# Kernel optimization log

Measured on AMD Instinct MI355X. Metric: run time of the kernel, lower is better.

The kernel has to match this reference:

```python
import jax, jax.numpy as jnp
import numpy as np

EPS = 1e-6          # VN leaky-relu denominator eps (vn_layers.py)
NEG_SLOPE = 0.2     # VNLinearLeakyReLU default negative_slope
K = 3               # pointops.interpolation default k
DIST_EPS = 1e-8     # interpolation inverse-distance eps


def vn_linear_leakyrelu(x, w_feat, w_dir):
    # x: [B, Cin, 3, N]; w_*: [Cout, Cin]  (bias-free Linears over channel dim)
    p = jnp.einsum('oc,bcvn->bovn', w_feat, x)
    d = jnp.einsum('oc,bcvn->bovn', w_dir, x)
    dot = jnp.sum(p * d, axis=2, keepdims=True)          # [B,Cout,1,N]
    d2 = jnp.sum(d * d, axis=2, keepdims=True)
    mask = (dot >= 0).astype(x.dtype)
    proj = p - (dot / (d2 + EPS)) * d                    # reflect negative part onto plane perp to d
    return NEG_SLOPE * p + (1.0 - NEG_SLOPE) * (mask * p + (1.0 - mask) * proj)


def interpolation(p2, p1, feat, b, n2, n1):
    # p2: [b*n2,3] coarse coords, p1: [b*n1,3] fine coords, feat: [C,3,b*n2]
    # k-NN inverse-squared-distance interpolation, segment-local per cloud.
    C = feat.shape[0]
    p2b = p2.reshape(b, n2, 3)
    p1b = p1.reshape(b, n1, 3)
    featb = feat.reshape(C * 3, b, n2).transpose(1, 2, 0)  # [b, n2, C*3]

    def per_batch(q, s, f):
        d2 = jnp.sum((q[:, None, :] - s[None, :, :]) ** 2, axis=-1)  # [n1,n2]
        neg_d2, idx = jax.lax.top_k(-d2, K)                          # k smallest sq-dists
        w = 1.0 / (-neg_d2 + DIST_EPS)
        w = w / jnp.sum(w, axis=1, keepdims=True)                    # [n1,K]
        return jnp.einsum('nk,nkc->nc', w, f[idx])                   # [n1, C*3]

    out = jax.vmap(per_batch)(p1b, p2b, featb)                       # [b, n1, C*3]
    return out.reshape(b, n1, C, 3).transpose(2, 3, 0, 1).reshape(C, 3, b * n1)


def setup_inputs() -> dict:
    key = jax.random.key(0)
    ks = jax.random.split(key, 8)
    b, n1, n2 = 4, 16384, 4096
    in_planes, out_planes = 128, 64
    p1 = jax.random.uniform(ks[0], (b * n1, 3), dtype=jnp.float32)
    p2 = jax.random.uniform(ks[1], (b * n2, 3), dtype=jnp.float32)
    x1 = jax.random.normal(ks[2], (1, out_planes, 3, b * n1), dtype=jnp.float32)
    x2 = jax.random.normal(ks[3], (1, in_planes, 3, b * n2), dtype=jnp.float32)
    o1 = (jnp.arange(1, b + 1, dtype=jnp.int32)) * n1   # cumulative offsets
    o2 = (jnp.arange(1, b + 1, dtype=jnp.int32)) * n2
    s1 = 1.0 / np.sqrt(out_planes)
    s2 = 1.0 / np.sqrt(in_planes)
    w1_feat = jax.random.uniform(ks[4], (out_planes, out_planes), jnp.float32, -s1, s1)
    w1_dir = jax.random.uniform(ks[5], (out_planes, out_planes), jnp.float32, -s1, s1)
    w2_feat = jax.random.uniform(ks[6], (out_planes, in_planes), jnp.float32, -s2, s2)
    w2_dir = jax.random.uniform(ks[7], (out_planes, in_planes), jnp.float32, -s2, s2)
    return {"p1": p1, "x1": x1, "o1": o1, "p2": p2, "x2": x2, "o2": o2,
            "w1_feat": w1_feat, "w1_dir": w1_dir, "w2_feat": w2_feat, "w2_dir": w2_dir}


def reference(p1, x1, o1, p2, x2, o2, w1_feat, w1_dir, w2_feat, w2_dir):
    b = o1.shape[0]
    n1 = x1.shape[-1] // b
    n2 = x2.shape[-1] // b
    y1 = vn_linear_leakyrelu(x1, w1_feat, w1_dir)            # [1,Cout,3,N1]
    y2 = vn_linear_leakyrelu(x2, w2_feat, w2_dir)[0]         # squeeze(0) -> [Cout,3,N2]
    up = interpolation(p2, p1, y2, b, n2, n1)                # [Cout,3,N1]
    return y1 + up
```

## Files before the change

### kernel.cpp

```cpp
#include <hip/hip_runtime.h>

#define N1T 65536
#define N2T 16384
#define COUT 64
#define CH 192
#define GRD 8
#define HCELL 0.125f

typedef unsigned short bhalf;
typedef __attribute__((ext_vector_type(8))) short short8;
typedef __attribute__((ext_vector_type(4))) float f32x4;

__device__ __forceinline__ bhalf f2bf(float f) {
    unsigned u = __float_as_uint(f);
    return (bhalf)((u + 0x7FFFu + ((u >> 16) & 1u)) >> 16);
}
__device__ __forceinline__ float bf2f(bhalf h) {
    return __uint_as_float(((unsigned)h) << 16);
}

__global__ __launch_bounds__(256) void prep_kernel(
    const float* __restrict__ w1f, const float* __restrict__ w1d,
    const float* __restrict__ w2f, const float* __restrict__ w2d,
    bhalf* __restrict__ o1fh, bhalf* __restrict__ o1fl,
    bhalf* __restrict__ o1dh, bhalf* __restrict__ o1dl,
    bhalf* __restrict__ o2fh, bhalf* __restrict__ o2fl,
    bhalf* __restrict__ o2dh, bhalf* __restrict__ o2dl,
    int* __restrict__ zp) {
    if (blockIdx.x < 32) {
        const int i = blockIdx.x * 256 + threadIdx.x;
        if (i < 4096) {
            const float a = w1f[i]; const bhalf ah = f2bf(a);
            o1fh[i] = ah; o1fl[i] = f2bf(a - bf2f(ah));
            const float b = w1d[i]; const bhalf bh = f2bf(b);
            o1dh[i] = bh; o1dl[i] = f2bf(b - bf2f(bh));
        }
        const float a = w2f[i]; const bhalf ah = f2bf(a);
        o2fh[i] = ah; o2fl[i] = f2bf(a - bf2f(ah));
        const float b = w2d[i]; const bhalf bh = f2bf(b);
        o2dh[i] = bh; o2dl[i] = f2bf(b - bf2f(bh));
    } else {
        const int i = (blockIdx.x - 32) * 256 + threadIdx.x;
        if (i < 4096) zp[i] = 0;
    }
}

template<int CIN, int N, bool CM, int NT>
__global__ __launch_bounds__(512) void vn_mfma_kernel(
    const float* __restrict__ x,
    const bhalf* __restrict__ wfh, const bhalf* __restrict__ wfl,
    const bhalf* __restrict__ wdh, const bhalf* __restrict__ wdl,
    const int*   __restrict__ idxs,
    const float* __restrict__ wts,
    const float* __restrict__ y2t,
    float* __restrict__ out)
{
    constexpr int ROWS = CIN * 3;
    constexpr int LDSC = CIN * 3 + 8;
    constexpr int NB   = (NT > 1) ? 2 : 1;
    constexpr int NLD  = ROWS * 8 / 512;
    __shared__ __align__(16) bhalf xs_h[NB][32][LDSC];
    __shared__ __align__(16) bhalf xs_l[NB][32][LDSC];

    const int tid  = threadIdx.x;
    const int lane = tid & 63;
    const int wave = tid >> 6;
    const int r16  = lane & 15;
    const int hh   = lane >> 4;
    const int ot   = wave & 3;
    const int sW   = wave >> 2;
    const int pt   = sW * 16 + r16;
    const int tile0 = blockIdx.x * NT;

    int gk[NT][3]; float gw[NT][3];
    if constexpr (CM) {
#pragma unroll
        for (int t = 0; t < NT; ++t) {
            const int n = (tile0 + t) * 32 + pt;
#pragma unroll
            for (int r = 0; r < 3; ++r) {
                gk[t][r] = idxs[r * N1T + n];
                gw[t][r] = wts[r * N1T + n];
            }
        }
    }

    const int wofs = (ot * 16 + r16) * CIN + hh * 8;
    const bhalf* __restrict__ pfh = wfh + wofs;
    const bhalf* __restrict__ pfl = wfl + wofs;
    const bhalf* __restrict__ pdh = wdh + wofs;
    const bhalf* __restrict__ pdl = wdl + wofs;
    const int hs = ((hh ^ (r16 >> 2)) & 3) * 8;

    auto LOADT = [&](float4 (&st)[NLD], int t) {
#pragma unroll
        for (int r = 0; r < NLD; ++r) {
            const int i4 = r * 512 + tid;
            const int row = i4 >> 3, p4 = i4 & 7;
            st[r] = *(const float4*)&x[(size_t)row * N + (size_t)(tile0 + t) * 32 + p4 * 4];
        }
    };
    auto WRITET = [&](const float4 (&st)[NLD], int b) {
#pragma unroll
        for (int r = 0; r < NLD; ++r) {
            const int i4 = r * 512 + tid;
            const int row = i4 >> 3, p4 = i4 & 7;
            const int c = row / 3, vv = row - c * 3;
            const int colS = (vv * CIN + c) ^ ((p4 & 3) << 3);
            const float vals[4] = {st[r].x, st[r].y, st[r].z, st[r].w};
#pragma unroll
            for (int j = 0; j < 4; ++j) {
                const bhalf h = f2bf(vals[j]);
                xs_h[b][p4*4+j][colS] = h;
                xs_l[b][p4*4+j][colS] = f2bf(vals[j] - bf2f(h));
            }
        }
    };
    auto COMPUTET = [&](int t, int b, const int (&gkt)[3], const float (&gwt)[3]) {
        const f32x4 zero = {0.f, 0.f, 0.f, 0.f};
        f32x4 accP[3], accD[3];
#pragma unroll
        for (int v = 0; v < 3; ++v) { accP[v] = zero; accD[v] = zero; }
#pragma unroll
        for (int k = 0; k < CIN / 32; ++k) {
            const short8 afh = *(const short8*)(pfh + k * 32);
            const short8 afl = *(const short8*)(pfl + k * 32);
            const short8 adh = *(const short8*)(pdh + k * 32);
            const short8 adl = *(const short8*)(pdl + k * 32);
#pragma unroll
            for (int v = 0; v < 3; ++v) {
                const short8 bh = *(const short8*)&xs_h[b][pt][v * CIN + k * 32 + hs];
                const short8 bl = *(const short8*)&xs_l[b][pt][v * CIN + k * 32 + hs];
                accP[v] = __builtin_amdgcn_mfma_f32_16x16x32_bf16(afh, bh, accP[v], 0, 0, 0);
                accP[v] = __builtin_amdgcn_mfma_f32_16x16x32_bf16(afl, bh, accP[v], 0, 0, 0);
                accP[v] = __builtin_amdgcn_mfma_f32_16x16x32_bf16(afh, bl, accP[v], 0, 0, 0);
                accD[v] = __builtin_amdgcn_mfma_f32_16x16x32_bf16(adh, bh, accD[v], 0, 0, 0);
                accD[v] = __builtin_amdgcn_mfma_f32_16x16x32_bf16(adl, bh, accD[v], 0, 0, 0);
                accD[v] = __builtin_amdgcn_mfma_f32_16x16x32_bf16(adh, bl, accD[v], 0, 0, 0);
            }
        }
        float rr[12];
#pragma unroll
        for (int reg = 0; reg < 4; ++reg) {
            const float p0 = accP[0][reg], p1 = accP[1][reg], p2 = accP[2][reg];
            const float q0 = accD[0][reg], q1 = accD[1][reg], q2 = accD[2][reg];
            const float dot = p0*q0 + p1*q1 + p2*q2;
            const float dd  = q0*q0 + q1*q1 + q2*q2;
            const float coef = (dot < 0.f) ? (0.8f * dot / (dd + 1e-6f)) : 0.f;
            rr[reg*3+0] = p0 - coef * q0;
            rr[reg*3+1] = p1 - coef * q1;
            rr[reg*3+2] = p2 - coef * q2;
        }
        const int n = (tile0 + t) * 32 + pt;
        if constexpr (!CM) {
            float* op = out + (size_t)n * CH + ot * 48 + hh * 12;
            *(float4*)&op[0] = make_float4(rr[0], rr[1], rr[2],  rr[3]);
            *(float4*)&op[4] = make_float4(rr[4], rr[5], rr[6],  rr[7]);
            *(float4*)&op[8] = make_float4(rr[8], rr[9], rr[10], rr[11]);
        } else {
            const int chb = ot * 48 + hh * 12;
            const float* __restrict__ r0 = y2t + (size_t)gkt[0] * CH + chb;
            const float* __restrict__ r1 = y2t + (size_t)gkt[1] * CH + chb;
            const float* __restrict__ r2 = y2t + (size_t)gkt[2] * CH + chb;
            const float w0 = gwt[0], w1 = gwt[1], w2 = gwt[2];
            float4 a0[3], a1[3], a2[3];
#pragma unroll
            for (int q = 0; q < 3; ++q) {
                a0[q] = *(const float4*)&r0[q * 4];
                a1[q] = *(const float4*)&r1[q * 4];
                a2[q] = *(const float4*)&r2[q * 4];
            }
#pragma unroll
            for (int q = 0; q < 3; ++q) {
                const float u0 = w0*a0[q].x + w1*a1[q].x + w2*a2[q].x;
                const float u1 = w0*a0[q].y + w1*a1[q].y + w2*a2[q].y;
                const float u2 = w0*a0[q].z + w1*a1[q].z + w2*a2[q].z;
                const float u3 = w0*a0[q].w + w1*a1[q].w + w2*a2[q].w;
                out[(size_t)(chb + q*4 + 0) * N + n] = rr[q*4+0] + u0;
                out[(size_t)(chb + q*4 + 1) * N + n] = rr[q*4+1] + u1;
                out[(size_t)(chb + q*4 + 2) * N + n] = rr[q*4+2] + u2;
                out[(size_t)(chb + q*4 + 3) * N + n] = rr[q*4+3] + u3;
            }
        }
    };

    float4 stA[NLD], stB[NLD];
    LOADT(stA, 0);
    WRITET(stA, 0);
    if constexpr (NT == 2) {
        LOADT(stB, 1);
        __syncthreads();
        COMPUTET(0, 0, gk[0], gw[0]);
        WRITET(stB, 1);
        __syncthreads();
        COMPUTET(1, 1, gk[1], gw[1]);
    } else {
        __syncthreads();
        COMPUTET(0, 0, gk[0], gw[0]);
    }
}

#define KNN_INSERT(d2, j)                                        \
    {                                                            \
        const bool c0 = (d2) < b0;                               \
        const bool c1 = (d2) < b1;                               \
        const bool c2 = (d2) < b2v;                              \
        const float nb2 = c2 ? (c1 ? b1 : (d2)) : b2v;           \
        const int   ni2 = c2 ? (c1 ? i1 : (j))  : i2;            \
        const float nb1 = c1 ? (c0 ? b0 : (d2)) : b1;            \
        const int   ni1 = c1 ? (c0 ? i0 : (j))  : i1;            \
        b0 = c0 ? (d2) : b0;  i0 = c0 ? (j) : i0;                \
        b1 = nb1; i1 = ni1; b2v = nb2; i2 = ni2;                 \
    }

__device__ __forceinline__ int cell_of(float x, float y, float z) {
    int cx = (int)(x * (float)GRD); cx = cx < 0 ? 0 : (cx > GRD-1 ? GRD-1 : cx);
    int cy = (int)(y * (float)GRD); cy = cy < 0 ? 0 : (cy > GRD-1 ? GRD-1 : cy);
    int cz = (int)(z * (float)GRD); cz = cz < 0 ? 0 : (cz > GRD-1 ? GRD-1 : cz);
    return (cz << 6) | (cy << 3) | cx;
}

__global__ __launch_bounds__(256) void bin_count_kernel(
    const float* __restrict__ p2, int* __restrict__ counts) {
    const int i = blockIdx.x * 256 + threadIdx.x;
    const float x = p2[i*3+0], y = p2[i*3+1], z = p2[i*3+2];
    const int cell = ((i >> 12) << 9) | cell_of(x, y, z);
    atomicAdd(&counts[cell], 1);
}

__global__ __launch_bounds__(256) void scan_kernel(
    const int* __restrict__ counts, int* __restrict__ off) {
    __shared__ int buf[2][256];
    const int t = threadIdx.x;
    int v[8]; int s = 0;
#pragma unroll
    for (int j = 0; j < 8; ++j) { const int tmp = counts[t*8+j]; v[j] = s; s += tmp; }
    buf[0][t] = s; __syncthreads();
    int src = 0;
    for (int d = 1; d < 256; d <<= 1) {
        int val = buf[src][t];
        if (t >= d) val += buf[src][t - d];
        buf[src ^ 1][t] = val; src ^= 1; __syncthreads();
    }
    const int incl = buf[src][t];
    const int base = incl - s;
#pragma unroll
    for (int j = 0; j < 8; ++j) off[t*8+j] = base + v[j];
    if (t == 255) off[2048] = incl;
}

__global__ __launch_bounds__(256) void bin_scatter_kernel(
    const float* __restrict__ p2, const int* __restrict__ off,
    int* __restrict__ cnt2, float4* __restrict__ binned) {
    const int i = blockIdx.x * 256 + threadIdx.x;
    const float x = p2[i*3+0], y = p2[i*3+1], z = p2[i*3+2];
    const int cell = ((i >> 12) << 9) | cell_of(x, y, z);
    const int pos = off[cell] + atomicAdd(&cnt2[cell], 1);
    binned[pos] = make_float4(x, y, z, __int_as_float(i));
}

__global__ __launch_bounds__(512) void vn2_knn_kernel(
    const float* __restrict__ x2,
    const bhalf* __restrict__ wfh, const bhalf* __restrict__ wfl,
    const bhalf* __restrict__ wdh, const bhalf* __restrict__ wdl,
    float* __restrict__ y2t,
    const float* __restrict__ p1,
    const float4* __restrict__ binned,
    const int* __restrict__ off,
    int*   __restrict__ idx_out,
    float* __restrict__ w_out)
{
    constexpr int CIN = 128, N = N2T;
    constexpr int LDSC = CIN * 3 + 8;
    __shared__ __align__(16) bhalf xs_h[32][LDSC];
    __shared__ __align__(16) bhalf xs_l[32][LDSC];

    const int role = blockIdx.x & 1;
    const int ridx = blockIdx.x >> 1;
    const int tid  = threadIdx.x;

    if (role == 0) {
        const int lane = tid & 63;
        const int wave = tid >> 6;
        const int r16  = lane & 15;
        const int hh   = lane >> 4;
        const int ot   = wave & 3;
        const int sW   = wave >> 2;
        const int pt   = sW * 16 + r16;
        const int n0   = ridx * 32;

        const int wofs = (ot * 16 + r16) * CIN + hh * 8;
        const bhalf* __restrict__ pfh = wfh + wofs;
        const bhalf* __restrict__ pfl = wfl + wofs;
        const bhalf* __restrict__ pdh = wdh + wofs;
        const bhalf* __restrict__ pdl = wdl + wofs;
        const int hs = ((hh ^ (r16 >> 2)) & 3) * 8;

#pragma unroll
        for (int r = 0; r < 6; ++r) {
            const int i4 = r * 512 + tid;
            const int row = i4 >> 3, p4 = i4 & 7;
            const float4 v = *(const float4*)&x2[(size_t)row * N + n0 + p4 * 4];
            const int c = row / 3, vv = row - c * 3;
            const int colS = (vv * CIN + c) ^ ((p4 & 3) << 3);
            const float vals[4] = {v.x, v.y, v.z, v.w};
#pragma unroll
            for (int j = 0; j < 4; ++j) {
                const bhalf h = f2bf(vals[j]);
                xs_h[p4*4+j][colS] = h;
                xs_l[p4*4+j][colS] = f2bf(vals[j] - bf2f(h));
            }
        }
        __syncthreads();

        const f32x4 zero = {0.f, 0.f, 0.f, 0.f};
        f32x4 accP[3], accD[3];
#pragma unroll
        for (int v = 0; v < 3; ++v) { accP[v] = zero; accD[v] = zero; }
#pragma unroll
        for (int k = 0; k < CIN / 32; ++k) {
            const short8 afh = *(const short8*)(pfh + k * 32);
            const short8 afl = *(const short8*)(pfl + k * 32);
            const short8 adh = *(const short8*)(pdh + k * 32);
            const short8 adl = *(const short8*)(pdl + k * 32);
#pragma unroll
            for (int v = 0; v < 3; ++v) {
                const short8 bh = *(const short8*)&xs_h[pt][v * CIN + k * 32 + hs];
                const short8 bl = *(const short8*)&xs_l[pt][v * CIN + k * 32 + hs];
                accP[v] = __builtin_amdgcn_mfma_f32_16x16x32_bf16(afh, bh, accP[v], 0, 0, 0);
                accP[v] = __builtin_amdgcn_mfma_f32_16x16x32_bf16(afl, bh, accP[v], 0, 0, 0);
                accP[v] = __builtin_amdgcn_mfma_f32_16x16x32_bf16(afh, bl, accP[v], 0, 0, 0);
                accD[v] = __builtin_amdgcn_mfma_f32_16x16x32_bf16(adh, bh, accD[v], 0, 0, 0);
                accD[v] = __builtin_amdgcn_mfma_f32_16x16x32_bf16(adl, bh, accD[v], 0, 0, 0);
                accD[v] = __builtin_amdgcn_mfma_f32_16x16x32_bf16(adh, bl, accD[v], 0, 0, 0);
            }
        }

        float rr[12];
#pragma unroll
        for (int reg = 0; reg < 4; ++reg) {
            const float p0 = accP[0][reg], p1 = accP[1][reg], p2 = accP[2][reg];
            const float q0 = accD[0][reg], q1 = accD[1][reg], q2 = accD[2][reg];
            const float dot = p0*q0 + p1*q1 + p2*q2;
            const float dd  = q0*q0 + q1*q1 + q2*q2;
            const float coef = (dot < 0.f) ? (0.8f * dot / (dd + 1e-6f)) : 0.f;
            rr[reg*3+0] = p0 - coef * q0;
            rr[reg*3+1] = p1 - coef * q1;
            rr[reg*3+2] = p2 - coef * q2;
        }
        const int n = n0 + pt;
        float* op = y2t + (size_t)n * CH + ot * 48 + hh * 12;
        *(float4*)&op[0] = make_float4(rr[0], rr[1], rr[2],  rr[3]);
        *(float4*)&op[4] = make_float4(rr[4], rr[5], rr[6],  rr[7]);
        *(float4*)&op[8] = make_float4(rr[8], rr[9], rr[10], rr[11]);
    } else {
        const int fp  = ridx * 128 + (tid >> 2);
        const int sub = tid & 3;
        const int bi  = fp >> 14;
        const int cbase = bi << 9;

        const float qx = p1[fp*3+0], qy = p1[fp*3+1], qz = p1[fp*3+2];
        int cx = (int)(qx * (float)GRD); cx = cx < 0 ? 0 : (cx > 7 ? 7 : cx);
        int cy = (int)(qy * (float)GRD); cy = cy < 0 ? 0 : (cy > 7 ? 7 : cy);
        int cz = (int)(qz * (float)GRD); cz = cz < 0 ? 0 : (cz > 7 ? 7 : cz);

        const int x0 = cx > 0 ? cx - 1 : 0;
        const int x1 = cx < 7 ? cx + 1 : 7;

        float b0 = 1e30f, b1 = 1e30f, b2v = 1e30f;
        int   i0 = 0,     i1 = 0,     i2 = 0;

#pragma unroll
        for (int dz = -1; dz <= 1; ++dz) {
            const int nz = cz + dz;
            if ((unsigned)nz > 7u) continue;
#pragma unroll
            for (int dy = -1; dy <= 1; ++dy) {
                const int ny = cy + dy;
                if ((unsigned)ny > 7u) continue;
                const int cb = cbase + (nz << 6) + (ny << 3);
                const int s = off[cb + x0], e = off[cb + x1 + 1];
                for (int k = s + sub; k < e; k += 4) {
                    const float4 c4 = binned[k];
                    const float ddx = qx - c4.x, ddy = qy - c4.y, ddz = qz - c4.z;
                    const float d2 = fmaf(ddx, ddx, fmaf(ddy, ddy, ddz * ddz));
                    const int j = __float_as_int(c4.w);
                    KNN_INSERT(d2, j)
                }
            }
        }

#pragma unroll
        for (int m = 1; m <= 2; m <<= 1) {
            const float c0v = __shfl_xor(b0, m, 4);
            const float c1v = __shfl_xor(b1, m, 4);
            const float c2v = __shfl_xor(b2v, m, 4);
            const int   j0v = __shfl_xor(i0, m, 4);
            const int   j1v = __shfl_xor(i1, m, 4);
            const int   j2v = __shfl_xor(i2, m, 4);
            KNN_INSERT(c0v, j0v)
            KNN_INSERT(c1v, j1v)
            KNN_INSERT(c2v, j2v)
        }

        float dw = 1e30f;
        if (cx >= 2) dw = fminf(dw, qx - (float)(cx - 1) * HCELL);
        if (cx <= 5) dw = fminf(dw, (float)(cx + 2) * HCELL - qx);
        if (cy >= 2) dw = fminf(dw, qy - (float)(cy - 1) * HCELL);
        if (cy <= 5) dw = fminf(dw, (float)(cy + 2) * HCELL - qy);
        if (cz >= 2) dw = fminf(dw, qz - (float)(cz - 1) * HCELL);
        if (cz <= 5) dw = fminf(dw, (float)(cz + 2) * HCELL - qz);
        const bool done = b2v < dw * dw;

        if (!done) {
            b0 = b1 = b2v = 1e30f; i0 = i1 = i2 = 0;
            const int s = bi << 12, e = (bi + 1) << 12;
            for (int k = s + sub; k < e; k += 4) {
                const float4 c4 = binned[k];
                const float ddx = qx - c4.x, ddy = qy - c4.y, ddz = qz - c4.z;
                const float d2 = fmaf(ddx, ddx, fmaf(ddy, ddy, ddz * ddz));
                const int j = __float_as_int(c4.w);
                KNN_INSERT(d2, j)
            }
#pragma unroll
            for (int m = 1; m <= 2; m <<= 1) {
                const float c0v = __shfl_xor(b0, m, 4);
                const float c1v = __shfl_xor(b1, m, 4);
                const float c2v = __shfl_xor(b2v, m, 4);
                const int   j0v = __shfl_xor(i0, m, 4);
                const int   j1v = __shfl_xor(i1, m, 4);
                const int   j2v = __shfl_xor(i2, m, 4);
                KNN_INSERT(c0v, j0v)
                KNN_INSERT(c1v, j1v)
                KNN_INSERT(c2v, j2v)
            }
        }

        if (sub == 0) {
            const float w0 = 1.f / (b0 + 1e-8f);
            const float w1 = 1.f / (b1 + 1e-8f);
            const float w2 = 1.f / (b2v + 1e-8f);
            const float inv = 1.f / (w0 + w1 + w2);
            idx_out[0*N1T + fp] = i0;
            idx_out[1*N1T + fp] = i1;
            idx_out[2*N1T + fp] = i2;
            w_out[0*N1T + fp] = w0 * inv;
            w_out[1*N1T + fp] = w1 * inv;
            w_out[2*N1T + fp] = w2 * inv;
        }
    }
}

extern "C" void kernel_launch(void* const* d_in, const int* in_sizes, int n_in,
                              void* d_out, int out_size, void* d_ws, size_t ws_size,
                              hipStream_t stream) {
    const float* p1      = (const float*)d_in[0];
    const float* x1      = (const float*)d_in[1];
    const float* p2      = (const float*)d_in[3];
    const float* x2      = (const float*)d_in[4];
    const float* w1_feat = (const float*)d_in[6];
    const float* w1_dir  = (const float*)d_in[7];
    const float* w2_feat = (const float*)d_in[8];
    const float* w2_dir  = (const float*)d_in[9];
    float* out = (float*)d_out;

    char* ws = (char*)d_ws;
    float*  y2t    = (float*)ws;                 ws += (size_t)N2T * CH * 4;
    int*    idxs   = (int*)ws;                   ws += (size_t)3 * N1T * 4;
    float*  wts    = (float*)ws;                 ws += (size_t)3 * N1T * 4;
    int*    counts = (int*)ws;                   ws += 2048 * 4;
    int*    cnt2   = (int*)ws;                   ws += 2048 * 4;
    int*    off    = (int*)ws;                   ws += 2064 * 4;
    float4* binned = (float4*)ws;                ws += (size_t)N2T * 16;
    bhalf*  wb1fh  = (bhalf*)ws;                 ws += 4096 * 2;
    bhalf*  wb1fl  = (bhalf*)ws;                 ws += 4096 * 2;
    bhalf*  wb1dh  = (bhalf*)ws;                 ws += 4096 * 2;
    bhalf*  wb1dl  = (bhalf*)ws;                 ws += 4096 * 2;
    bhalf*  wb2fh  = (bhalf*)ws;                 ws += 8192 * 2;
    bhalf*  wb2fl  = (bhalf*)ws;                 ws += 8192 * 2;
    bhalf*  wb2dh  = (bhalf*)ws;                 ws += 8192 * 2;
    bhalf*  wb2dl  = (bhalf*)ws;                 ws += 8192 * 2;

    prep_kernel<<<48, 256, 0, stream>>>(w1_feat, w1_dir, w2_feat, w2_dir,
                                        wb1fh, wb1fl, wb1dh, wb1dl,
                                        wb2fh, wb2fl, wb2dh, wb2dl, counts);
    bin_count_kernel<<<N2T/256, 256, 0, stream>>>(p2, counts);
    scan_kernel<<<1, 256, 0, stream>>>(counts, off);
    bin_scatter_kernel<<<N2T/256, 256, 0, stream>>>(p2, off, cnt2, binned);
    vn2_knn_kernel<<<1024, 512, 0, stream>>>(
        x2, wb2fh, wb2fl, wb2dh, wb2dl, y2t,
        p1, binned, off, idxs, wts);
    vn_mfma_kernel<64, N1T, true, 2><<<N1T/64, 512, 0, stream>>>(
        x1, wb1fh, wb1fl, wb1dh, wb1dl, idxs, wts, y2t, out);
}
```

Measured before the change: 98.95 us.

## Split VN2 and kNN into separate kernels and shrink VN1 tile to 16 points

Result: no change. 99.27 us (+0.3%).

```diff
diff --git a/kernel.cpp b/kernel.cpp
--- a/kernel.cpp
+++ b/kernel.cpp
@@ -19,34 +19,28 @@
     return __uint_as_float(((unsigned)h) << 16);
 }
 
-__global__ __launch_bounds__(256) void prep_kernel(
+__global__ __launch_bounds__(256) void wconv_kernel(
     const float* __restrict__ w1f, const float* __restrict__ w1d,
     const float* __restrict__ w2f, const float* __restrict__ w2d,
     bhalf* __restrict__ o1fh, bhalf* __restrict__ o1fl,
     bhalf* __restrict__ o1dh, bhalf* __restrict__ o1dl,
     bhalf* __restrict__ o2fh, bhalf* __restrict__ o2fl,
-    bhalf* __restrict__ o2dh, bhalf* __restrict__ o2dl,
-    int* __restrict__ zp) {
-    if (blockIdx.x < 32) {
-        const int i = blockIdx.x * 256 + threadIdx.x;
-        if (i < 4096) {
-            const float a = w1f[i]; const bhalf ah = f2bf(a);
-            o1fh[i] = ah; o1fl[i] = f2bf(a - bf2f(ah));
-            const float b = w1d[i]; const bhalf bh = f2bf(b);
-            o1dh[i] = bh; o1dl[i] = f2bf(b - bf2f(bh));
-        }
-        const float a = w2f[i]; const bhalf ah = f2bf(a);
-        o2fh[i] = ah; o2fl[i] = f2bf(a - bf2f(ah));
-        const float b = w2d[i]; const bhalf bh = f2bf(b);
-        o2dh[i] = bh; o2dl[i] = f2bf(b - bf2f(bh));
-    } else {
-        const int i = (blockIdx.x - 32) * 256 + threadIdx.x;
-        if (i < 4096) zp[i] = 0;
-    }
-}
-
-template<int CIN, int N, bool CM, int NT>
-__global__ __launch_bounds__(512) void vn_mfma_kernel(
+    bhalf* __restrict__ o2dh, bhalf* __restrict__ o2dl) {
+    const int i = blockIdx.x * 256 + threadIdx.x;
+    if (i < 4096) {
+        const float a = w1f[i]; const bhalf ah = f2bf(a);
+        o1fh[i] = ah; o1fl[i] = f2bf(a - bf2f(ah));
+        const float b = w1d[i]; const bhalf bh = f2bf(b);
+        o1dh[i] = bh; o1dl[i] = f2bf(b - bf2f(bh));
+    }
+    const float a = w2f[i]; const bhalf ah = f2bf(a);
+    o2fh[i] = ah; o2fl[i] = f2bf(a - bf2f(ah));
+    const float b = w2d[i]; const bhalf bh = f2bf(b);
+    o2dh[i] = bh; o2dl[i] = f2bf(b - bf2f(bh));
+}
+
+template<int N>
+__global__ __launch_bounds__(256) void vn1_fused16_kernel(
     const float* __restrict__ x,
     const bhalf* __restrict__ wfh, const bhalf* __restrict__ wfl,
     const bhalf* __restrict__ wdh, const bhalf* __restrict__ wdl,
@@ -55,33 +49,27 @@
     const float* __restrict__ y2t,
     float* __restrict__ out)
 {
-    constexpr int ROWS = CIN * 3;
-    constexpr int LDSC = CIN * 3 + 8;
-    constexpr int NB   = (NT > 1) ? 2 : 1;
-    constexpr int NLD  = ROWS * 8 / 512;
-    __shared__ __align__(16) bhalf xs_h[NB][32][LDSC];
-    __shared__ __align__(16) bhalf xs_l[NB][32][LDSC];
+    constexpr int CIN  = 64;
+    constexpr int LDSC = 200;
+    __shared__ __align__(16) bhalf xs_h[2][16][LDSC];
+    __shared__ __align__(16) bhalf xs_l[2][16][LDSC];
 
     const int tid  = threadIdx.x;
     const int lane = tid & 63;
-    const int wave = tid >> 6;
+    const int ot   = tid >> 6;
     const int r16  = lane & 15;
     const int hh   = lane >> 4;
-    const int ot   = wave & 3;
-    const int sW   = wave >> 2;
-    const int pt   = sW * 16 + r16;
-    const int tile0 = blockIdx.x * NT;
-
-    int gk[NT][3]; float gw[NT][3];
-    if constexpr (CM) {
-#pragma unroll
-        for (int t = 0; t < NT; ++t) {
-            const int n = (tile0 + t) * 32 + pt;
-#pragma unroll
-            for (int r = 0; r < 3; ++r) {
-                gk[t][r] = idxs[r * N1T + n];
-                gw[t][r] = wts[r * N1T + n];
-            }
+    const int tile0 = blockIdx.x * 2;
+    const int chb  = ot * 48 + hh * 12;
+
+    int gk[2][3]; float gw[2][3];
+#pragma unroll
+    for (int t = 0; t < 2; ++t) {
+        const int n = (tile0 + t) * 16 + r16;
+#pragma unroll
+        for (int r = 0; r < 3; ++r) {
+            gk[t][r] = idxs[r * N1T + n];
+            gw[t][r] = wts[r * N1T + n];
         }
     }
 
@@ -92,21 +80,21 @@
     const bhalf* __restrict__ pdl = wdl + wofs;
     const int hs = ((hh ^ (r16 >> 2)) & 3) * 8;
 
-    auto LOADT = [&](float4 (&st)[NLD], int t) {
-#pragma unroll
-        for (int r = 0; r < NLD; ++r) {
-            const int i4 = r * 512 + tid;
-            const int row = i4 >> 3, p4 = i4 & 7;
-            st[r] = *(const float4*)&x[(size_t)row * N + (size_t)(tile0 + t) * 32 + p4 * 4];
+    auto LOADT = [&](float4 (&st)[3], int t) {
+#pragma unroll
+        for (int r = 0; r < 3; ++r) {
+            const int i4 = r * 256 + tid;
+            const int row = i4 >> 2, p4 = i4 & 3;
+            st[r] = *(const float4*)&x[(size_t)row * N + (size_t)(tile0 + t) * 16 + p4 * 4];
         }
     };
-    auto WRITET = [&](const float4 (&st)[NLD], int b) {
-#pragma unroll
-        for (int r = 0; r < NLD; ++r) {
-            const int i4 = r * 512 + tid;
-            const int row = i4 >> 3, p4 = i4 & 7;
+    auto WRITET = [&](const float4 (&st)[3], int b) {
+#pragma unroll
+        for (int r = 0; r < 3; ++r) {
+            const int i4 = r * 256 + tid;
+            const int row = i4 >> 2, p4 = i4 & 3;
             const int c = row / 3, vv = row - c * 3;
-            const int colS = (vv * CIN + c) ^ ((p4 & 3) << 3);
+            const int colS = (vv * CIN + c) ^ (p4 << 3);
             const float vals[4] = {st[r].x, st[r].y, st[r].z, st[r].w};
 #pragma unroll
             for (int j = 0; j < 4; ++j) {
@@ -122,15 +110,15 @@
 #pragma unroll
         for (int v = 0; v < 3; ++v) { accP[v] = zero; accD[v] = zero; }
 #pragma unroll
-        for (int k = 0; k < CIN / 32; ++k) {
+        for (int k = 0; k < 2; ++k) {
             const short8 afh = *(const short8*)(pfh + k * 32);
             const short8 afl = *(const short8*)(pfl + k * 32);
             const short8 adh = *(const short8*)(pdh + k * 32);
             const short8 adl = *(const short8*)(pdl + k * 32);
 #pragma unroll
             for (int v = 0; v < 3; ++v) {
-                const short8 bh = *(const short8*)&xs_h[b][pt][v * CIN + k * 32 + hs];
-                const short8 bl = *(const short8*)&xs_l[b][pt][v * CIN + k * 32 + hs];
+                const short8 bh = *(const short8*)&xs_h[b][r16][v * CIN + k * 32 + hs];
+                const short8 bl = *(const short8*)&xs_l[b][r16][v * CIN + k * 32 + hs];
                 accP[v] = __builtin_amdgcn_mfma_f32_16x16x32_bf16(afh, bh, accP[v], 0, 0, 0);
                 accP[v] = __builtin_amdgcn_mfma_f32_16x16x32_bf16(afl, bh, accP[v], 0, 0, 0);
                 accP[v] = __builtin_amdgcn_mfma_f32_16x16x32_bf16(afh, bl, accP[v], 0, 0, 0);
@@ -151,53 +139,129 @@
             rr[reg*3+1] = p1 - coef * q1;
             rr[reg*3+2] = p2 - coef * q2;
         }
-        const int n = (tile0 + t) * 32 + pt;
-        if constexpr (!CM) {
-            float* op = out + (size_t)n * CH + ot * 48 + hh * 12;
-            *(float4*)&op[0] = make_float4(rr[0], rr[1], rr[2],  rr[3]);
-            *(float4*)&op[4] = make_float4(rr[4], rr[5], rr[6],  rr[7]);
-            *(float4*)&op[8] = make_float4(rr[8], rr[9], rr[10], rr[11]);
-        } else {
-            const int chb = ot * 48 + hh * 12;
-            const float* __restrict__ r0 = y2t + (size_t)gkt[0] * CH + chb;
-            const float* __restrict__ r1 = y2t + (size_t)gkt[1] * CH + chb;
-            const float* __restrict__ r2 = y2t + (size_t)gkt[2] * CH + chb;
-            const float w0 = gwt[0], w1 = gwt[1], w2 = gwt[2];
-            float4 a0[3], a1[3], a2[3];
-#pragma unroll
-            for (int q = 0; q < 3; ++q) {
-                a0[q] = *(const float4*)&r0[q * 4];
-                a1[q] = *(const float4*)&r1[q * 4];
-                a2[q] = *(const float4*)&r2[q * 4];
-            }
-#pragma unroll
-            for (int q = 0; q < 3; ++q) {
-                const float u0 = w0*a0[q].x + w1*a1[q].x + w2*a2[q].x;
-                const float u1 = w0*a0[q].y + w1*a1[q].y + w2*a2[q].y;
-                const float u2 = w0*a0[q].z + w1*a1[q].z + w2*a2[q].z;
-                const float u3 = w0*a0[q].w + w1*a1[q].w + w2*a2[q].w;
-                out[(size_t)(chb + q*4 + 0) * N + n] = rr[q*4+0] + u0;
-                out[(size_t)(chb + q*4 + 1) * N + n] = rr[q*4+1] + u1;
-                out[(size_t)(chb + q*4 + 2) * N + n] = rr[q*4+2] + u2;
-                out[(size_t)(chb + q*4 + 3) * N + n] = rr[q*4+3] + u3;
-            }
+        const int n = (tile0 + t) * 16 + r16;
+        const float* __restrict__ r0 = y2t + (size_t)gkt[0] * CH + chb;
+        const float* __restrict__ r1 = y2t + (size_t)gkt[1] * CH + chb;
+        const float* __restrict__ r2 = y2t + (size_t)gkt[2] * CH + chb;
+        const float w0 = gwt[0], w1 = gwt[1], w2 = gwt[2];
+        float4 a0[3], a1[3], a2[3];
+#pragma unroll
+        for (int q = 0; q < 3; ++q) {
+            a0[q] = *(const float4*)&r0[q * 4];
+            a1[q] = *(const float4*)&r1[q * 4];
+            a2[q] = *(const float4*)&r2[q * 4];
+        }
+#pragma unroll
+        for (int q = 0; q < 3; ++q) {
+            const float u0 = w0*a0[q].x + w1*a1[q].x + w2*a2[q].x;
+            const float u1 = w0*a0[q].y + w1*a1[q].y + w2*a2[q].y;
+            const float u2 = w0*a0[q].z + w1*a1[q].z + w2*a2[q].z;
+            const float u3 = w0*a0[q].w + w1*a1[q].w + w2*a2[q].w;
+            out[(size_t)(chb + q*4 + 0) * N + n] = rr[q*4+0] + u0;
+            out[(size_t)(chb + q*4 + 1) * N + n] = rr[q*4+1] + u1;
+            out[(size_t)(chb + q*4 + 2) * N + n] = rr[q*4+2] + u2;
+            out[(size_t)(chb + q*4 + 3) * N + n] = rr[q*4+3] + u3;
         }
     };
 
-    float4 stA[NLD], stB[NLD];
+    float4 stA[3], stB[3];
     LOADT(stA, 0);
     WRITET(stA, 0);
-    if constexpr (NT == 2) {
-        LOADT(stB, 1);
-        __syncthreads();
-        COMPUTET(0, 0, gk[0], gw[0]);
-        WRITET(stB, 1);
-        __syncthreads();
-        COMPUTET(1, 1, gk[1], gw[1]);
-    } else {
-        __syncthreads();
-        COMPUTET(0, 0, gk[0], gw[0]);
-    }
+    LOADT(stB, 1);
+    __syncthreads();
+    COMPUTET(0, 0, gk[0], gw[0]);
+    WRITET(stB, 1);
+    __syncthreads();
+    COMPUTET(1, 1, gk[1], gw[1]);
+}
+
+template<int CIN, int N>
+__global__ __launch_bounds__(512) void vn_mfma_kernel(
+    const float* __restrict__ x,
+    const bhalf* __restrict__ wfh, const bhalf* __restrict__ wfl,
+    const bhalf* __restrict__ wdh, const bhalf* __restrict__ wdl,
+    float* __restrict__ out)
+{
+    constexpr int ROWS = CIN * 3;
+    constexpr int LDSC = CIN * 3 + 8;
+    constexpr int NLD  = ROWS * 8 / 512;
+    __shared__ __align__(16) bhalf xs_h[32][LDSC];
+    __shared__ __align__(16) bhalf xs_l[32][LDSC];
+
+    const int tid  = threadIdx.x;
+    const int lane = tid & 63;
+    const int wave = tid >> 6;
+    const int r16  = lane & 15;
+    const int hh   = lane >> 4;
+    const int ot   = wave & 3;
+    const int sW   = wave >> 2;
+    const int pt   = sW * 16 + r16;
+    const int n0   = blockIdx.x * 32;
+
+    const int wofs = (ot * 16 + r16) * CIN + hh * 8;
+    const bhalf* __restrict__ pfh = wfh + wofs;
+    const bhalf* __restrict__ pfl = wfl + wofs;
+    const bhalf* __restrict__ pdh = wdh + wofs;
+    const bhalf* __restrict__ pdl = wdl + wofs;
+    const int hs = ((hh ^ (r16 >> 2)) & 3) * 8;
+
+#pragma unroll
+    for (int r = 0; r < NLD; ++r) {
+        const int i4 = r * 512 + tid;
+        const int row = i4 >> 3, p4 = i4 & 7;
+        const float4 v = *(const float4*)&x[(size_t)row * N + n0 + p4 * 4];
+        const int c = row / 3, vv = row - c * 3;
+        const int colS = (vv * CIN + c) ^ ((p4 & 3) << 3);
+        const float vals[4] = {v.x, v.y, v.z, v.w};
+#pragma unroll
+        for (int j = 0; j < 4; ++j) {
+            const bhalf h = f2bf(vals[j]);
+            xs_h[p4*4+j][colS] = h;
+            xs_l[p4*4+j][colS] = f2bf(vals[j] - bf2f(h));
+        }
+    }
+    __syncthreads();
+
+    const f32x4 zero = {0.f, 0.f, 0.f, 0.f};
+    f32x4 accP[3], accD[3];
+#pragma unroll
+    for (int v = 0; v < 3; ++v) { accP[v] = zero; accD[v] = zero; }
+#pragma unroll
+    for (int k = 0; k < CIN / 32; ++k) {
+        const short8 afh = *(const short8*)(pfh + k * 32);
+        const short8 afl = *(const short8*)(pfl + k * 32);
+        const short8 adh = *(const short8*)(pdh + k * 32);
+        const short8 adl = *(const short8*)(pdl + k * 32);
+#pragma unroll
+        for (int v = 0; v < 3; ++v) {
+            const short8 bh = *(const short8*)&xs_h[pt][v * CIN + k * 32 + hs];
+            const short8 bl = *(const short8*)&xs_l[pt][v * CIN + k * 32 + hs];
+            accP[v] = __builtin_amdgcn_mfma_f32_16x16x32_bf16(afh, bh, accP[v], 0, 0, 0);
+            accP[v] = __builtin_amdgcn_mfma_f32_16x16x32_bf16(afl, bh, accP[v], 0, 0, 0);
+            accP[v] = __builtin_amdgcn_mfma_f32_16x16x32_bf16(afh, bl, accP[v], 0, 0, 0);
+            accD[v] = __builtin_amdgcn_mfma_f32_16x16x32_bf16(adh, bh, accD[v], 0, 0, 0);
+            accD[v] = __builtin_amdgcn_mfma_f32_16x16x32_bf16(adl, bh, accD[v], 0, 0, 0);
+            accD[v] = __builtin_amdgcn_mfma_f32_16x16x32_bf16(adh, bl, accD[v], 0, 0, 0);
+        }
+    }
+
+    float rr[12];
+#pragma unroll
+    for (int reg = 0; reg < 4; ++reg) {
+        const float p0 = accP[0][reg], p1 = accP[1][reg], p2 = accP[2][reg];
+        const float q0 = accD[0][reg], q1 = accD[1][reg], q2 = accD[2][reg];
+        const float dot = p0*q0 + p1*q1 + p2*q2;
+        const float dd  = q0*q0 + q1*q1 + q2*q2;
+        const float coef = (dot < 0.f) ? (0.8f * dot / (dd + 1e-6f)) : 0.f;
+        rr[reg*3+0] = p0 - coef * q0;
+        rr[reg*3+1] = p1 - coef * q1;
+        rr[reg*3+2] = p2 - coef * q2;
+    }
+    const int n = n0 + pt;
+    float* op = out + (size_t)n * CH + ot * 48 + hh * 12;
+    *(float4*)&op[0] = make_float4(rr[0], rr[1], rr[2],  rr[3]);
+    *(float4*)&op[4] = make_float4(rr[4], rr[5], rr[6],  rr[7]);
+    *(float4*)&op[8] = make_float4(rr[8], rr[9], rr[10], rr[11]);
 }
 
 #define KNN_INSERT(d2, j)                                        \
@@ -213,6 +277,11 @@
         b1 = nb1; i1 = ni1; b2v = nb2; i2 = ni2;                 \
     }
 
+__global__ __launch_bounds__(256) void zero_kernel(int* __restrict__ p, int n) {
+    const int i = blockIdx.x * 256 + threadIdx.x;
+    if (i < n) p[i] = 0;
+}
+
 __device__ __forceinline__ int cell_of(float x, float y, float z) {
     int cx = (int)(x * (float)GRD); cx = cx < 0 ? 0 : (cx > GRD-1 ? GRD-1 : cx);
     int cy = (int)(y * (float)GRD); cy = cy < 0 ? 0 : (cy > GRD-1 ? GRD-1 : cy);
@@ -259,137 +328,82 @@
     binned[pos] = make_float4(x, y, z, __int_as_float(i));
 }
 
-__global__ __launch_bounds__(512) void vn2_knn_kernel(
-    const float* __restrict__ x2,
-    const bhalf* __restrict__ wfh, const bhalf* __restrict__ wfl,
-    const bhalf* __restrict__ wdh, const bhalf* __restrict__ wdl,
-    float* __restrict__ y2t,
+__global__ __launch_bounds__(256) void knn_grid_kernel(
     const float* __restrict__ p1,
     const float4* __restrict__ binned,
     const int* __restrict__ off,
     int*   __restrict__ idx_out,
     float* __restrict__ w_out)
 {
-    constexpr int CIN = 128, N = N2T;
-    constexpr int LDSC = CIN * 3 + 8;
-    __shared__ __align__(16) bhalf xs_h[32][LDSC];
-    __shared__ __align__(16) bhalf xs_l[32][LDSC];
-
-    const int role = blockIdx.x & 1;
-    const int ridx = blockIdx.x >> 1;
-    const int tid  = threadIdx.x;
-
-    if (role == 0) {
-        const int lane = tid & 63;
-        const int wave = tid >> 6;
-        const int r16  = lane & 15;
-        const int hh   = lane >> 4;
-        const int ot   = wave & 3;
-        const int sW   = wave >> 2;
-        const int pt   = sW * 16 + r16;
-        const int n0   = ridx * 32;
-
-        const int wofs = (ot * 16 + r16) * CIN + hh * 8;
-        const bhalf* __restrict__ pfh = wfh + wofs;
-        const bhalf* __restrict__ pfl = wfl + wofs;
-        const bhalf* __restrict__ pdh = wdh + wofs;
-        const bhalf* __restrict__ pdl = wdl + wofs;
-        const int hs = ((hh ^ (r16 >> 2)) & 3) * 8;
-
-#pragma unroll
-        for (int r = 0; r < 6; ++r) {
-            const int i4 = r * 512 + tid;
-            const int row = i4 >> 3, p4 = i4 & 7;
-            const float4 v = *(const float4*)&x2[(size_t)row * N + n0 + p4 * 4];
-            const int c = row / 3, vv = row - c * 3;
-            const int colS = (vv * CIN + c) ^ ((p4 & 3) << 3);
-            const float vals[4] = {v.x, v.y, v.z, v.w};
-#pragma unroll
-            for (int j = 0; j < 4; ++j) {
-                const bhalf h = f2bf(vals[j]);
-                xs_h[p4*4+j][colS] = h;
-                xs_l[p4*4+j][colS] = f2bf(vals[j] - bf2f(h));
+    const int t   = blockIdx.x * 256 + threadIdx.x;
+    const int fp  = t >> 2;
+    const int sub = t & 3;
+    const int bi  = fp >> 14;
+    const int cbase = bi << 9;
+
+    const float qx = p1[fp*3+0], qy = p1[fp*3+1], qz = p1[fp*3+2];
+    int cx = (int)(qx * (float)GRD); cx = cx < 0 ? 0 : (cx > 7 ? 7 : cx);
+    int cy = (int)(qy * (float)GRD); cy = cy < 0 ? 0 : (cy > 7 ? 7 : cy);
+    int cz = (int)(qz * (float)GRD); cz = cz < 0 ? 0 : (cz > 7 ? 7 : cz);
+
+    const int x0 = cx > 0 ? cx - 1 : 0;
+    const int x1 = cx < 7 ? cx + 1 : 7;
+
+    float b0 = 1e30f, b1 = 1e30f, b2v = 1e30f;
+    int   i0 = 0,     i1 = 0,     i2 = 0;
+
+#pragma unroll
+    for (int dz = -1; dz <= 1; ++dz) {
+        const int nz = cz + dz;
+        if ((unsigned)nz > 7u) continue;
+#pragma unroll
+        for (int dy = -1; dy <= 1; ++dy) {
+            const int ny = cy + dy;
+            if ((unsigned)ny > 7u) continue;
+            const int cb = cbase + (nz << 6) + (ny << 3);
+            const int s = off[cb + x0], e = off[cb + x1 + 1];
+            for (int k = s + sub; k < e; k += 4) {
+                const float4 c4 = binned[k];
+                const float ddx = qx - c4.x, ddy = qy - c4.y, ddz = qz - c4.z;
+                const float d2 = fmaf(ddx, ddx, fmaf(ddy, ddy, ddz * ddz));
+                const int j = __float_as_int(c4.w);
+                KNN_INSERT(d2, j)
             }
         }
-        __syncthreads();
-
-        const f32x4 zero = {0.f, 0.f, 0.f, 0.f};
-        f32x4 accP[3], accD[3];
-#pragma unroll
-        for (int v = 0; v < 3; ++v) { accP[v] = zero; accD[v] = zero; }
-#pragma unroll
-        for (int k = 0; k < CIN / 32; ++k) {
-            const short8 afh = *(const short8*)(pfh + k * 32);
-            const short8 afl = *(const short8*)(pfl + k * 32);
-            const short8 adh = *(const short8*)(pdh + k * 32);
-            const short8 adl = *(const short8*)(pdl + k * 32);
-#pragma unroll
-            for (int v = 0; v < 3; ++v) {
-                const short8 bh = *(const short8*)&xs_h[pt][v * CIN + k * 32 + hs];
-                const short8 bl = *(const short8*)&xs_l[pt][v * CIN + k * 32 + hs];
-                accP[v] = __builtin_amdgcn_mfma_f32_16x16x32_bf16(afh, bh, accP[v], 0, 0, 0);
-                accP[v] = __builtin_amdgcn_mfma_f32_16x16x32_bf16(afl, bh, accP[v], 0, 0, 0);
-                accP[v] = __builtin_amdgcn_mfma_f32_16x16x32_bf16(afh, bl, accP[v], 0, 0, 0);
-                accD[v] = __builtin_amdgcn_mfma_f32_16x16x32_bf16(adh, bh, accD[v], 0, 0, 0);
-                accD[v] = __builtin_amdgcn_mfma_f32_16x16x32_bf16(adl, bh, accD[v], 0, 0, 0);
-                accD[v] = __builtin_amdgcn_mfma_f32_16x16x32_bf16(adh, bl, accD[v], 0, 0, 0);
-            }
-        }
-
-        float rr[12];
-#pragma unroll
-        for (int reg = 0; reg < 4; ++reg) {
-            const float p0 = accP[0][reg], p1 = accP[1][reg], p2 = accP[2][reg];
-            const float q0 = accD[0][reg], q1 = accD[1][reg], q2 = accD[2][reg];
-            const float dot = p0*q0 + p1*q1 + p2*q2;
-            const float dd  = q0*q0 + q1*q1 + q2*q2;
-            const float coef = (dot < 0.f) ? (0.8f * dot / (dd + 1e-6f)) : 0.f;
-            rr[reg*3+0] = p0 - coef * q0;
-            rr[reg*3+1] = p1 - coef * q1;
-            rr[reg*3+2] = p2 - coef * q2;
-        }
-        const int n = n0 + pt;
-        float* op = y2t + (size_t)n * CH + ot * 48 + hh * 12;
-        *(float4*)&op[0] = make_float4(rr[0], rr[1], rr[2],  rr[3]);
-        *(float4*)&op[4] = make_float4(rr[4], rr[5], rr[6],  rr[7]);
-        *(float4*)&op[8] = make_float4(rr[8], rr[9], rr[10], rr[11]);
-    } else {
-        const int fp  = ridx * 128 + (tid >> 2);
-        const int sub = tid & 3;
-        const int bi  = fp >> 14;
-        const int cbase = bi << 9;
-
-        const float qx = p1[fp*3+0], qy = p1[fp*3+1], qz = p1[fp*3+2];
-        int cx = (int)(qx * (float)GRD); cx = cx < 0 ? 0 : (cx > 7 ? 7 : cx);
-        int cy = (int)(qy * (float)GRD); cy = cy < 0 ? 0 : (cy > 7 ? 7 : cy);
-        int cz = (int)(qz * (float)GRD); cz = cz < 0 ? 0 : (cz > 7 ? 7 : cz);
-
-        const int x0 = cx > 0 ? cx - 1 : 0;
-        const int x1 = cx < 7 ? cx + 1 : 7;
-
-        float b0 = 1e30f, b1 = 1e30f, b2v = 1e30f;
-        int   i0 = 0,     i1 = 0,     i2 = 0;
-
-#pragma unroll
-        for (int dz = -1; dz <= 1; ++dz) {
-            const int nz = cz + dz;
-            if ((unsigned)nz > 7u) continue;
-#pragma unroll
-            for (int dy = -1; dy <= 1; ++dy) {
-                const int ny = cy + dy;
-                if ((unsigned)ny > 7u) continue;
-                const int cb = cbase + (nz << 6) + (ny << 3);
-                const int s = off[cb + x0], e = off[cb + x1 + 1];
-                for (int k = s + sub; k < e; k += 4) {
-                    const float4 c4 = binned[k];
-                    const float ddx = qx - c4.x, ddy = qy - c4.y, ddz = qz - c4.z;
-                    const float d2 = fmaf(ddx, ddx, fmaf(ddy, ddy, ddz * ddz));
-                    const int j = __float_as_int(c4.w);
-                    KNN_INSERT(d2, j)
-                }
-            }
-        }
-
+    }
+
+#pragma unroll
+    for (int m = 1; m <= 2; m <<= 1) {
+        const float c0v = __shfl_xor(b0, m, 4);
+        const float c1v = __shfl_xor(b1, m, 4);
+        const float c2v = __shfl_xor(b2v, m, 4);
+        const int   j0v = __shfl_xor(i0, m, 4);
+        const int   j1v = __shfl_xor(i1, m, 4);
+        const int   j2v = __shfl_xor(i2, m, 4);
+        KNN_INSERT(c0v, j0v)
+        KNN_INSERT(c1v, j1v)
+        KNN_INSERT(c2v, j2v)
+    }
+
+    float dw = 1e30f;
+    if (cx >= 2) dw = fminf(dw, qx - (float)(cx - 1) * HCELL);
+    if (cx <= 5) dw = fminf(dw, (float)(cx + 2) * HCELL - qx);
+    if (cy >= 2) dw = fminf(dw, qy - (float)(cy - 1) * HCELL);
+    if (cy <= 5) dw = fminf(dw, (float)(cy + 2) * HCELL - qy);
+    if (cz >= 2) dw = fminf(dw, qz - (float)(cz - 1) * HCELL);
+    if (cz <= 5) dw = fminf(dw, (float)(cz + 2) * HCELL - qz);
+    const bool done = b2v < dw * dw;
+
+    if (!done) {
+        b0 = b1 = b2v = 1e30f; i0 = i1 = i2 = 0;
+        const int s = bi << 12, e = (bi + 1) << 12;
+        for (int k = s + sub; k < e; k += 4) {
+            const float4 c4 = binned[k];
+            const float ddx = qx - c4.x, ddy = qy - c4.y, ddz = qz - c4.z;
+            const float d2 = fmaf(ddx, ddx, fmaf(ddy, ddy, ddz * ddz));
+            const int j = __float_as_int(c4.w);
+            KNN_INSERT(d2, j)
+        }
 #pragma unroll
         for (int m = 1; m <= 2; m <<= 1) {
             const float c0v = __shfl_xor(b0, m, 4);
@@ -402,52 +416,19 @@
             KNN_INSERT(c1v, j1v)
             KNN_INSERT(c2v, j2v)
         }
-
-        float dw = 1e30f;
-        if (cx >= 2) dw = fminf(dw, qx - (float)(cx - 1) * HCELL);
-        if (cx <= 5) dw = fminf(dw, (float)(cx + 2) * HCELL - qx);
-        if (cy >= 2) dw = fminf(dw, qy - (float)(cy - 1) * HCELL);
-        if (cy <= 5) dw = fminf(dw, (float)(cy + 2) * HCELL - qy);
-        if (cz >= 2) dw = fminf(dw, qz - (float)(cz - 1) * HCELL);
-        if (cz <= 5) dw = fminf(dw, (float)(cz + 2) * HCELL - qz);
-        const bool done = b2v < dw * dw;
-
-        if (!done) {
-            b0 = b1 = b2v = 1e30f; i0 = i1 = i2 = 0;
-            const int s = bi << 12, e = (bi + 1) << 12;
-            for (int k = s + sub; k < e; k += 4) {
-                const float4 c4 = binned[k];
-                const float ddx = qx - c4.x, ddy = qy - c4.y, ddz = qz - c4.z;
-                const float d2 = fmaf(ddx, ddx, fmaf(ddy, ddy, ddz * ddz));
-                const int j = __float_as_int(c4.w);
-                KNN_INSERT(d2, j)
-            }
-#pragma unroll
-            for (int m = 1; m <= 2; m <<= 1) {
-                const float c0v = __shfl_xor(b0, m, 4);
-                const float c1v = __shfl_xor(b1, m, 4);
-                const float c2v = __shfl_xor(b2v, m, 4);
-                const int   j0v = __shfl_xor(i0, m, 4);
-                const int   j1v = __shfl_xor(i1, m, 4);
-                const int   j2v = __shfl_xor(i2, m, 4);
-                KNN_INSERT(c0v, j0v)
-                KNN_INSERT(c1v, j1v)
-                KNN_INSERT(c2v, j2v)
-            }
-        }
-
-        if (sub == 0) {
-            const float w0 = 1.f / (b0 + 1e-8f);
-            const float w1 = 1.f / (b1 + 1e-8f);
-            const float w2 = 1.f / (b2v + 1e-8f);
-            const float inv = 1.f / (w0 + w1 + w2);
-            idx_out[0*N1T + fp] = i0;
-            idx_out[1*N1T + fp] = i1;
-            idx_out[2*N1T + fp] = i2;
-            w_out[0*N1T + fp] = w0 * inv;
-            w_out[1*N1T + fp] = w1 * inv;
-            w_out[2*N1T + fp] = w2 * inv;
-        }
+    }
+
+    if (sub == 0) {
+        const float w0 = 1.f / (b0 + 1e-8f);
+        const float w1 = 1.f / (b1 + 1e-8f);
+        const float w2 = 1.f / (b2v + 1e-8f);
+        const float inv = 1.f / (w0 + w1 + w2);
+        idx_out[0*N1T + fp] = i0;
+        idx_out[1*N1T + fp] = i1;
+        idx_out[2*N1T + fp] = i2;
+        w_out[0*N1T + fp] = w0 * inv;
+        w_out[1*N1T + fp] = w1 * inv;
+        w_out[2*N1T + fp] = w2 * inv;
     }
 }
 
@@ -481,15 +462,19 @@
     bhalf*  wb2dh  = (bhalf*)ws;                 ws += 8192 * 2;
     bhalf*  wb2dl  = (bhalf*)ws;                 ws += 8192 * 2;
 
-    prep_kernel<<<48, 256, 0, stream>>>(w1_feat, w1_dir, w2_feat, w2_dir,
-                                        wb1fh, wb1fl, wb1dh, wb1dl,
-                                        wb2fh, wb2fl, wb2dh, wb2dl, counts);
+    wconv_kernel<<<32, 256, 0, stream>>>(w1_feat, w1_dir, w2_feat, w2_dir,
+                                         wb1fh, wb1fl, wb1dh, wb1dl,
+                                         wb2fh, wb2fl, wb2dh, wb2dl);
+
+    zero_kernel<<<16, 256, 0, stream>>>(counts, 4096);
     bin_count_kernel<<<N2T/256, 256, 0, stream>>>(p2, counts);
     scan_kernel<<<1, 256, 0, stream>>>(counts, off);
     bin_scatter_kernel<<<N2T/256, 256, 0, stream>>>(p2, off, cnt2, binned);
-    vn2_knn_kernel<<<1024, 512, 0, stream>>>(
-        x2, wb2fh, wb2fl, wb2dh, wb2dl, y2t,
-        p1, binned, off, idxs, wts);
-    vn_mfma_kernel<64, N1T, true, 2><<<N1T/64, 512, 0, stream>>>(
+    knn_grid_kernel<<<(4*N1T)/256, 256, 0, stream>>>(p1, binned, off, idxs, wts);
+
+    vn_mfma_kernel<128, N2T><<<N2T/32, 512, 0, stream>>>(
+        x2, wb2fh, wb2fl, wb2dh, wb2dl, y2t);
+
+    vn1_fused16_kernel<N1T><<<N1T/32, 256, 0, stream>>>(
         x1, wb1fh, wb1fl, wb1dh, wb1dl, idxs, wts, y2t, out);
 }
```
